# Kernel tuning notes

Measured on AMD Instinct MI355X. Metric: run time of the kernel, lower is better.

The kernel has to match this reference:

```python
import jax, jax.numpy as jnp
import numpy as np

HIDDEN = 1024
HEADS = 16
HEAD = HIDDEN // HEADS


def setup_inputs() -> dict:
    key = jax.random.key(0)
    ks = jax.random.split(key, 5)
    s = 1.0 / np.sqrt(HIDDEN)
    return {
        "x": jax.random.normal(ks[0], (32, 512, HIDDEN), dtype=jnp.float32),
        "w_qkv": jax.random.uniform(ks[1], (HIDDEN, 3 * HIDDEN), jnp.float32, -s, s),
        "b_qkv": jax.random.uniform(ks[2], (3 * HIDDEN,), jnp.float32, -s, s),
        "w_out": jax.random.uniform(ks[3], (HIDDEN, HIDDEN), jnp.float32, -s, s),
        "b_out": jax.random.uniform(ks[4], (HIDDEN,), jnp.float32, -s, s),
    }


def reference(x, w_qkv, b_qkv, w_out, b_out):
    bv, p, _ = x.shape
    qkv = x @ w_qkv + b_qkv                       # [bv, p, 3*hidden]
    qkv = qkv.reshape(bv, p, 3, HEADS, HEAD)
    q, k, v = qkv[:, :, 0], qkv[:, :, 1], qkv[:, :, 2]  # [bv, p, h, d]
    # scaled dot-product attention per head (dropout = identity in eval)
    scores = jnp.einsum("bqhd,bkhd->bhqk", q, k) / np.sqrt(HEAD).astype(np.float32)
    probs = jax.nn.softmax(scores, axis=-1)
    z = jnp.einsum("bhqk,bkhd->bqhd", probs, v).reshape(bv, p, HIDDEN)
    return z @ w_out + b_out
```

## Files before the change

### kernel.cpp

```cpp
#include <hip/hip_runtime.h>
#include <stdint.h>

#define KDIM 1024

typedef float  f32x4  __attribute__((ext_vector_type(4)));
typedef short  bf16x8 __attribute__((ext_vector_type(8)));
typedef unsigned short u16;
typedef unsigned int   u32;
typedef u16    u16x8  __attribute__((ext_vector_type(8)));

__device__ __forceinline__ float b2f(u16 u){ u32 x = ((u32)u)<<16; return __builtin_bit_cast(float, x); }
__device__ __forceinline__ u16  f2b(float f){
  u32 u = __builtin_bit_cast(u32, f);
  return (u16)((u + 0x7fffu + ((u>>16)&1u))>>16);
}
__device__ __forceinline__ u32 pk2(float a, float b){ return (u32)f2b(a) | ((u32)f2b(b)<<16); }

__device__ __forceinline__ void gload16(const void* g, void* l){
  __builtin_amdgcn_global_load_lds(
      (const __attribute__((address_space(1))) void*)g,
      (__attribute__((address_space(3))) void*)l, 16, 0, 0);
}

__global__ void k_cvt(const float* __restrict__ in, u16* __restrict__ out, int n8){
  int i = blockIdx.x*256 + threadIdx.x;
  if (i >= n8) return;
  const float4* p = (const float4*)in + (i<<1);
  float4 a = p[0], b = p[1];
  u16x8 o;
  o[0]=f2b(a.x); o[1]=f2b(a.y); o[2]=f2b(a.z); o[3]=f2b(a.w);
  o[4]=f2b(b.x); o[5]=f2b(b.y); o[6]=f2b(b.z); o[7]=f2b(b.w);
  *((u16x8*)out + i) = o;
}

__global__ void k_cvtT(const float* __restrict__ in, u16* __restrict__ out, int R, int C){
  __shared__ float t[32][33];
  int tx = threadIdx.x & 31, ty = threadIdx.x >> 5;
  int c0 = blockIdx.x<<5, r0 = blockIdx.y<<5;
  #pragma unroll
  for (int j=0;j<32;j+=8) t[ty+j][tx] = in[(r0+ty+j)*C + c0+tx];
  __syncthreads();
  #pragma unroll
  for (int j=0;j<32;j+=8) out[(c0+ty+j)*R + r0+tx] = f2b(t[tx][ty+j]);
}

template<int EPI>
__global__ __launch_bounds__(256, 3) void k_gemm(const u16* __restrict__ A, const u16* __restrict__ Bt,
    const float* __restrict__ bias, u16* __restrict__ oq, u16* __restrict__ ok2, u16* __restrict__ ov,
    float* __restrict__ of)
{
  __shared__ u16 lA[128*64];
  __shared__ u16 lB[128*64];
  const int t = threadIdx.x, lane = t & 63, wid = t >> 6;
  const int l15 = lane & 15, g = lane >> 4;
  const int m0 = blockIdx.y << 7, n0 = blockIdx.x << 7;
  const int wr = wid >> 1, wc = wid & 1;
  const f32x4 fz = {0.f,0.f,0.f,0.f};
  f32x4 acc[4][4];
  #pragma unroll
  for (int m=0;m<4;m++)
    #pragma unroll
    for (int n=0;n<4;n++) acc[m][n] = fz;

  for (int kt = 0; kt < KDIM; kt += 64) {
    __syncthreads();
    #pragma unroll
    for (int i=0;i<4;i++){
      int s = (i<<8) + t;
      int row = s >> 3;
      int c8 = (s & 7) ^ (row & 7);
      gload16(A + (m0 + row)*KDIM + kt + (c8<<3), (char*)lA + (((i<<2) + wid)<<10));
    }
    #pragma unroll
    for (int i=0;i<4;i++){
      int s = (i<<8) + t;
      int row = s >> 3;
      int c8 = (s & 7) ^ (row & 7);
      gload16(Bt + (n0 + row)*KDIM + kt + (c8<<3), (char*)lB + (((i<<2) + wid)<<10));
    }
    __syncthreads();
    #pragma unroll
    for (int ks=0; ks<2; ++ks){
      const int c8 = (ks<<2) + g;
      bf16x8 af[4], bfr[4];
      #pragma unroll
      for (int m=0;m<4;m++){
        int row = (wr<<6) + (m<<4) + l15;
        af[m] = *(const bf16x8*)((const char*)lA + (row<<7) + ((c8 ^ (row&7))<<4));
      }
      #pragma unroll
      for (int n=0;n<4;n++){
        int row = (wc<<6) + (n<<4) + l15;
        bfr[n] = *(const bf16x8*)((const char*)lB + (row<<7) + ((c8 ^ (row&7))<<4));
      }
      #pragma unroll
      for (int m=0;m<4;m++)
        #pragma unroll
        for (int n=0;n<4;n++)
          acc[m][n] = __builtin_amdgcn_mfma_f32_16x16x32_bf16(af[m], bfr[n], acc[m][n], 0,0,0);
    }
  }

  if (EPI == 0) {
    const int which = n0 >> 10;
    u16* dst = (which==0) ? oq : (which==1) ? ok2 : ov;
    #pragma unroll
    for (int n=0;n<4;n++){
      int n_g = n0 + (wc<<6) + (n<<4) + l15;
      float bv = bias[n_g];
      int h = (n_g >> 6) & 15, d = n_g & 63;
      #pragma unroll
      for (int m=0;m<4;m++){
        int mg = m0 + (wr<<6) + (m<<4) + (g<<2);
        #pragma unroll
        for (int j=0;j<4;j++){
          int m_g = mg + j;
          int bb = m_g >> 9, p = m_g & 511;
          dst[((bb*16 + h)*512 + p)*64 + d] = f2b(acc[m][n][j] + bv);
        }
      }
    }
  } else {
    #pragma unroll
    for (int n=0;n<4;n++){
      int n_g = n0 + (wc<<6) + (n<<4) + l15;
      float bv = bias[n_g];
      #pragma unroll
      for (int m=0;m<4;m++){
        int mg = m0 + (wr<<6) + (m<<4) + (g<<2);
        #pragma unroll
        for (int j=0;j<4;j++)
          of[(mg+j)*1024 + n_g] = acc[m][n][j] + bv;
      }
    }
  }
}

__global__ void k_vt(const u16* __restrict__ v, u16* __restrict__ vt){
  __shared__ u16 tl[64][65];
  const int bh = blockIdx.y, p0 = blockIdx.x << 6;
  const int t = threadIdx.x;
  #pragma unroll
  for (int i=0;i<4;i++){
    int e4 = (i<<8) + t;
    int r = e4 >> 4, c = (e4 & 15) << 2;
    ushort4 x = *(const ushort4*)&v[((bh<<9) + p0 + r)*64 + c];
    tl[r][c+0]=x.x; tl[r][c+1]=x.y; tl[r][c+2]=x.z; tl[r][c+3]=x.w;
  }
  __syncthreads();
  #pragma unroll
  for (int i=0;i<4;i++){
    int e4 = (i<<8) + t;
    int d = e4 >> 4, c = (e4 & 15) << 2;
    ushort4 x;
    x.x = tl[c+0][d]; x.y = tl[c+1][d]; x.z = tl[c+2][d]; x.w = tl[c+3][d];
    *(ushort4*)&vt[((bh<<6) + d)*512 + p0 + c] = x;
  }
}

__global__ __launch_bounds__(256, 2) void k_attn(const u16* __restrict__ q, const u16* __restrict__ k,
                                                 const u16* __restrict__ vt, u16* __restrict__ z)
{
  __shared__ u16 lK[64*64];
  __shared__ u16 lV[64*64];
  __shared__ u16 lP[4][64*64];
  const int t = threadIdx.x, lane = t & 63, wid = t >> 6;
  const int l15 = lane & 15, g = lane >> 4;
  const int bh = blockIdx.x >> 1, qt = blockIdx.x & 1;
  const int bb = bh >> 4, h = bh & 15;
  const int q0 = (qt<<8) + (wid<<6);
  const float cs = 0.18033688011112042f;

  bf16x8 qf[4][2];
  #pragma unroll
  for (int mf=0; mf<4; mf++)
    #pragma unroll
    for (int ks=0; ks<2; ks++){
      bf16x8 vq = *(const bf16x8*)(q + ((bh<<9) + q0 + (mf<<4) + l15)*64 + (ks<<5) + (g<<3));
      #pragma unroll
      for (int j=0;j<8;j++) vq[j] = (short)f2b(b2f((u16)vq[j]) * cs);
      qf[mf][ks] = vq;
    }

  const f32x4 fz = {0.f,0.f,0.f,0.f};
  f32x4 zt[4][4];
  #pragma unroll
  for (int df=0;df<4;df++)
    #pragma unroll
    for (int mf=0;mf<4;mf++) zt[df][mf] = fz;
  float mrun[4], lrun[4];
  #pragma unroll
  for (int mf=0;mf<4;mf++){ mrun[mf] = -__builtin_inff(); lrun[mf] = 0.f; }

  for (int kv0 = 0; kv0 < 512; kv0 += 64) {
    __syncthreads();
    #pragma unroll
    for (int i=0;i<2;i++){
      int s = (i<<8) + t;
      int row = s >> 3;
      int c8 = (s & 7) ^ (row & 7);
      gload16(k  + ((bh<<9) + kv0 + row)*64 + (c8<<3), (char*)lK + (((i<<2)+wid)<<10));
    }
    #pragma unroll
    for (int i=0;i<2;i++){
      int s = (i<<8) + t;
      int row = s >> 3;
      int c8 = (s & 7) ^ (row & 7);
      gload16(vt + ((bh<<6) + row)*512 + kv0 + (c8<<3), (char*)lV + (((i<<2)+wid)<<10));
    }
    __syncthreads();

    f32x4 sc[4][4];
    #pragma unroll
    for (int nf=0;nf<4;nf++)
      #pragma unroll
      for (int mf=0;mf<4;mf++) sc[nf][mf] = fz;
    #pragma unroll
    for (int ks=0; ks<2; ks++){
      const int c8 = (ks<<2) + g;
      bf16x8 kf[4];
      #pragma unroll
      for (int nf=0;nf<4;nf++){
        int row = (nf<<4) + l15;
        kf[nf] = *(const bf16x8*)((const char*)lK + (row<<7) + ((c8 ^ (row&7))<<4));
      }
      #pragma unroll
      for (int nf=0;nf<4;nf++)
        #pragma unroll
        for (int mf=0;mf<4;mf++)
          sc[nf][mf] = __builtin_amdgcn_mfma_f32_16x16x32_bf16(kf[nf], qf[mf][ks], sc[nf][mf], 0,0,0);
    }

    #pragma unroll
    for (int mf=0;mf<4;mf++){
      float pm = -__builtin_inff();
      #pragma unroll
      for (int nf=0;nf<4;nf++)
        #pragma unroll
        for (int j=0;j<4;j++) pm = fmaxf(pm, sc[nf][mf][j]);
      pm = fmaxf(pm, __shfl_xor(pm, 16));
      pm = fmaxf(pm, __shfl_xor(pm, 32));
      float mnew = fmaxf(mrun[mf], pm);
      float corr = __builtin_amdgcn_exp2f(mrun[mf] - mnew);
      mrun[mf] = mnew;
      float rs = 0.f;
      #pragma unroll
      for (int nf=0;nf<4;nf++)
        #pragma unroll
        for (int j=0;j<4;j++){
          float pv = __builtin_amdgcn_exp2f(sc[nf][mf][j] - mnew);
          sc[nf][mf][j] = pv; rs += pv;
        }
      rs += __shfl_xor(rs, 16);
      rs += __shfl_xor(rs, 32);
      lrun[mf] = lrun[mf]*corr + rs;
      #pragma unroll
      for (int df=0;df<4;df++){
        zt[df][mf][0]*=corr; zt[df][mf][1]*=corr; zt[df][mf][2]*=corr; zt[df][mf][3]*=corr;
      }
    }

    #pragma unroll
    for (int nf=0;nf<4;nf++)
      #pragma unroll
      for (int mf=0;mf<4;mf++){
        int qr = (mf<<4) + l15;
        int c8 = (nf<<1) + (g>>1);
        uint2 w2; w2.x = pk2(sc[nf][mf][0], sc[nf][mf][1]);
        w2.y = pk2(sc[nf][mf][2], sc[nf][mf][3]);
        *(uint2*)((char*)lP[wid] + (qr<<7) + ((c8 ^ (qr&7))<<4) + ((g&1)<<3)) = w2;
      }
    asm volatile("s_waitcnt lgkmcnt(0)" ::: "memory");

    #pragma unroll
    for (int ks=0; ks<2; ks++){
      const int c8 = (ks<<2) + g;
      bf16x8 vf[4], pf[4];
      #pragma unroll
      for (int df=0;df<4;df++){
        int row = (df<<4) + l15;
        vf[df] = *(const bf16x8*)((const char*)lV + (row<<7) + ((c8 ^ (row&7))<<4));
      }
      #pragma unroll
      for (int mf=0;mf<4;mf++){
        int qr = (mf<<4) + l15;
        pf[mf] = *(const bf16x8*)((const char*)lP[wid] + (qr<<7) + ((c8 ^ (qr&7))<<4));
      }
      #pragma unroll
      for (int df=0;df<4;df++)
        #pragma unroll
        for (int mf=0;mf<4;mf++)
          zt[df][mf] = __builtin_amdgcn_mfma_f32_16x16x32_bf16(vf[df], pf[mf], zt[df][mf], 0,0,0);
    }
  }

  #pragma unroll
  for (int mf=0;mf<4;mf++){
    float inv = 1.0f / lrun[mf];
    int qr = (mf<<4) + l15;
    int pg = (qt<<8) + (wid<<6) + qr;
    #pragma unroll
    for (int df=0;df<4;df++){
      int d0 = (df<<4) + (g<<2);
      ushort4 o;
      o.x = f2b(zt[df][mf][0]*inv);
      o.y = f2b(zt[df][mf][1]*inv);
      o.z = f2b(zt[df][mf][2]*inv);
      o.w = f2b(zt[df][mf][3]*inv);
      *(ushort4*)&z[ (((bb<<9) + pg)*16 + h)*64 + d0 ] = o;
    }
  }
}

extern "C" void kernel_launch(void* const* d_in, const int* in_sizes, int n_in,
                              void* d_out, int out_size, void* d_ws, size_t ws_size,
                              hipStream_t stream)
{
  (void)in_sizes; (void)n_in; (void)out_size; (void)ws_size;
  const float* x    = (const float*)d_in[0];
  const float* wqkv = (const float*)d_in[1];
  const float* bqkv = (const float*)d_in[2];
  const float* wout = (const float*)d_in[3];
  const float* bout = (const float*)d_in[4];
  float* out = (float*)d_out;
  char* w = (char*)d_ws;

  u16* wqT = (u16*)(w + 0);
  u16* woT = (u16*)(w + 6291456);
  u16* xb  = (u16*)(w + 8388608);
  u16* vtb = xb;
  u16* qb  = (u16*)(w + 41943040);
  u16* kb  = (u16*)(w + 75497472);
  u16* vb  = (u16*)(w + 109051904);
  u16* zb  = vb;

  k_cvt <<<dim3(8192),    dim3(256), 0, stream>>>(x, xb, 2097152);
  k_cvtT<<<dim3(96, 32),  dim3(256), 0, stream>>>(wqkv, wqT, 1024, 3072);
  k_cvtT<<<dim3(32, 32),  dim3(256), 0, stream>>>(wout, woT, 1024, 1024);
  k_gemm<0><<<dim3(24, 128), dim3(256), 0, stream>>>(xb, wqT, bqkv, qb, kb, vb, nullptr);
  k_vt  <<<dim3(8, 512),  dim3(256), 0, stream>>>(vb, vtb);
  k_attn<<<dim3(1024),    dim3(256), 0, stream>>>(qb, kb, vtb, zb);
  k_gemm<1><<<dim3(8, 128), dim3(256), 0, stream>>>(zb, woT, bout, nullptr, nullptr, nullptr, out);
}
```

Before: 377.4 us.

## Rewrite GEMM as 256x256 tile, 8-wave, double-buffered pipelined kernel

```diff
diff --git a/kernel.cpp b/kernel.cpp
--- a/kernel.cpp
+++ b/kernel.cpp
@@ -20,6 +20,14 @@
   __builtin_amdgcn_global_load_lds(
       (const __attribute__((address_space(1))) void*)g,
       (__attribute__((address_space(3))) void*)l, 16, 0, 0);
+}
+
+__device__ __forceinline__ void phase_bar(){
+  __builtin_amdgcn_sched_barrier(0);
+  asm volatile("s_waitcnt lgkmcnt(0)" ::: "memory");
+  __builtin_amdgcn_sched_barrier(0);
+  __builtin_amdgcn_s_barrier();
+  __builtin_amdgcn_sched_barrier(0);
 }
 
 __global__ void k_cvt(const float* __restrict__ in, u16* __restrict__ out, int n8){
@@ -44,93 +52,179 @@
   for (int j=0;j<32;j+=8) out[(c0+ty+j)*R + r0+tx] = f2b(t[tx][ty+j]);
 }
 
+__device__ __forceinline__ void stage2(const u16* __restrict__ src, int rowbase, int kt,
+                                       u16* lbuf, int grp0, int grp1, int lane){
+  int r7 = lane >> 3;
+  int c8 = (lane & 7) ^ r7;
+  const u16* s0 = src + (size_t)(rowbase + (grp0<<3) + r7)*KDIM + kt + (c8<<3);
+  const u16* s1 = src + (size_t)(rowbase + (grp1<<3) + r7)*KDIM + kt + (c8<<3);
+  gload16(s0, (char*)lbuf + (grp0<<10));
+  gload16(s1, (char*)lbuf + (grp1<<10));
+}
+
 template<int EPI>
-__global__ __launch_bounds__(256, 3) void k_gemm(const u16* __restrict__ A, const u16* __restrict__ Bt,
+__global__ __launch_bounds__(512, 2) void k_gemm(const u16* __restrict__ A, const u16* __restrict__ Bt,
     const float* __restrict__ bias, u16* __restrict__ oq, u16* __restrict__ ok2, u16* __restrict__ ov,
-    float* __restrict__ of)
+    float* __restrict__ of, int ntn)
 {
-  __shared__ u16 lA[128*64];
-  __shared__ u16 lB[128*64];
+  __shared__ u16 ldsb[2][2][256*64];
   const int t = threadIdx.x, lane = t & 63, wid = t >> 6;
   const int l15 = lane & 15, g = lane >> 4;
-  const int m0 = blockIdx.y << 7, n0 = blockIdx.x << 7;
-  const int wr = wid >> 1, wc = wid & 1;
+  const int wr = wid >> 2, wc = wid & 3;
+
+  const int nwg = gridDim.x, cpx = nwg >> 3, bid = blockIdx.x;
+  const int swz = (bid & 7)*cpx + (bid >> 3);
+  const int mt = swz / ntn, nt = swz % ntn;
+  const int m0 = mt << 8, n0 = nt << 8;
+
   const f32x4 fz = {0.f,0.f,0.f,0.f};
-  f32x4 acc[4][4];
-  #pragma unroll
-  for (int m=0;m<4;m++)
+  f32x4 acc[8][4];
+  #pragma unroll
+  for (int m=0;m<8;m++)
     #pragma unroll
     for (int n=0;n<4;n++) acc[m][n] = fz;
 
-  for (int kt = 0; kt < KDIM; kt += 64) {
-    __syncthreads();
-    #pragma unroll
-    for (int i=0;i<4;i++){
-      int s = (i<<8) + t;
-      int row = s >> 3;
-      int c8 = (s & 7) ^ (row & 7);
-      gload16(A + (m0 + row)*KDIM + kt + (c8<<3), (char*)lA + (((i<<2) + wid)<<10));
-    }
-    #pragma unroll
-    for (int i=0;i<4;i++){
-      int s = (i<<8) + t;
-      int row = s >> 3;
-      int c8 = (s & 7) ^ (row & 7);
-      gload16(Bt + (n0 + row)*KDIM + kt + (c8<<3), (char*)lB + (((i<<2) + wid)<<10));
-    }
-    __syncthreads();
-    #pragma unroll
-    for (int ks=0; ks<2; ++ks){
-      const int c8 = (ks<<2) + g;
-      bf16x8 af[4], bfr[4];
-      #pragma unroll
-      for (int m=0;m<4;m++){
-        int row = (wr<<6) + (m<<4) + l15;
-        af[m] = *(const bf16x8*)((const char*)lA + (row<<7) + ((c8 ^ (row&7))<<4));
-      }
-      #pragma unroll
-      for (int n=0;n<4;n++){
-        int row = (wc<<6) + (n<<4) + l15;
-        bfr[n] = *(const bf16x8*)((const char*)lB + (row<<7) + ((c8 ^ (row&7))<<4));
-      }
-      #pragma unroll
-      for (int m=0;m<4;m++)
-        #pragma unroll
-        for (int n=0;n<4;n++)
-          acc[m][n] = __builtin_amdgcn_mfma_f32_16x16x32_bf16(af[m], bfr[n], acc[m][n], 0,0,0);
-    }
+  const int NT = KDIM / 64;
+  const int sb0g0 = (wid<4)? wid    : wid+4;
+  const int sb0g1 = (wid<4)? wid+16 : wid+20;
+  const int sb1g0 = sb0g0 + 4, sb1g1 = sb0g1 + 4;
+
+  stage2(A,  m0, 0,  ldsb[0][0], wid,   wid+16, lane);
+  stage2(A,  m0, 0,  ldsb[0][0], wid+8, wid+24, lane);
+  stage2(Bt, n0, 0,  ldsb[0][1], sb0g0, sb0g1,  lane);
+  stage2(Bt, n0, 0,  ldsb[0][1], sb1g0, sb1g1,  lane);
+  stage2(A,  m0, 64, ldsb[1][0], wid,   wid+16, lane);
+  stage2(Bt, n0, 64, ldsb[1][1], sb0g0, sb0g1,  lane);
+  stage2(Bt, n0, 64, ldsb[1][1], sb1g0, sb1g1,  lane);
+  __builtin_amdgcn_sched_barrier(0);
+  asm volatile("s_waitcnt vmcnt(6) lgkmcnt(0)" ::: "memory");
+  __builtin_amdgcn_sched_barrier(0);
+  __builtin_amdgcn_s_barrier();
+  __builtin_amdgcn_sched_barrier(0);
+
+  for (int tt = 0; tt < NT; ++tt) {
+    const int b = tt & 1;
+    const char* cA = (const char*)ldsb[b][0];
+    const char* cB = (const char*)ldsb[b][1];
+    u16* nA1 = ldsb[b^1][0];
+    u16* nA2 = ldsb[b][0];
+    u16* nB2 = ldsb[b][1];
+    const int kt1 = (tt+1) << 6, kt2 = (tt+2) << 6;
+
+    bf16x8 af[4][2], b0[2][2], b1[2][2];
+
+    if (tt + 1 < NT) stage2(A, m0, kt1, nA1, wid+8, wid+24, lane);
+    #pragma unroll
+    for (int mf=0; mf<4; mf++)
+      #pragma unroll
+      for (int ks=0; ks<2; ks++){
+        int row = (wr<<7) + (mf<<4) + l15, c8 = (ks<<2) + g;
+        af[mf][ks] = *(const bf16x8*)(cA + (row<<7) + ((c8 ^ (row&7))<<4));
+      }
+    #pragma unroll
+    for (int nf=0; nf<2; nf++)
+      #pragma unroll
+      for (int ks=0; ks<2; ks++){
+        int row = (wc<<6) + (nf<<4) + l15, c8 = (ks<<2) + g;
+        b0[nf][ks] = *(const bf16x8*)(cB + (row<<7) + ((c8 ^ (row&7))<<4));
+      }
+    __builtin_amdgcn_s_setprio(1);
+    #pragma unroll
+    for (int mf=0; mf<4; mf++)
+      #pragma unroll
+      for (int nf=0; nf<2; nf++)
+        #pragma unroll
+        for (int ks=0; ks<2; ks++)
+          acc[mf][nf] = __builtin_amdgcn_mfma_f32_16x16x32_bf16(af[mf][ks], b0[nf][ks], acc[mf][nf], 0,0,0);
+    __builtin_amdgcn_s_setprio(0);
+    phase_bar();
+
+    if (tt + 2 < NT) stage2(A, m0, kt2, nA2, wid, wid+16, lane);
+    #pragma unroll
+    for (int nf=0; nf<2; nf++)
+      #pragma unroll
+      for (int ks=0; ks<2; ks++){
+        int row = (wc<<6) + ((nf+2)<<4) + l15, c8 = (ks<<2) + g;
+        b1[nf][ks] = *(const bf16x8*)(cB + (row<<7) + ((c8 ^ (row&7))<<4));
+      }
+    __builtin_amdgcn_s_setprio(1);
+    #pragma unroll
+    for (int mf=0; mf<4; mf++)
+      #pragma unroll
+      for (int nf=0; nf<2; nf++)
+        #pragma unroll
+        for (int ks=0; ks<2; ks++)
+          acc[mf][nf+2] = __builtin_amdgcn_mfma_f32_16x16x32_bf16(af[mf][ks], b1[nf][ks], acc[mf][nf+2], 0,0,0);
+    __builtin_amdgcn_s_setprio(0);
+    phase_bar();
+
+    if (tt + 2 < NT) stage2(Bt, n0, kt2, nB2, sb0g0, sb0g1, lane);
+    #pragma unroll
+    for (int mf=0; mf<4; mf++)
+      #pragma unroll
+      for (int ks=0; ks<2; ks++){
+        int row = (wr<<7) + ((mf+4)<<4) + l15, c8 = (ks<<2) + g;
+        af[mf][ks] = *(const bf16x8*)(cA + (row<<7) + ((c8 ^ (row&7))<<4));
+      }
+    __builtin_amdgcn_s_setprio(1);
+    #pragma unroll
+    for (int mf=0; mf<4; mf++)
+      #pragma unroll
+      for (int nf=0; nf<2; nf++)
+        #pragma unroll
+        for (int ks=0; ks<2; ks++)
+          acc[mf+4][nf] = __builtin_amdgcn_mfma_f32_16x16x32_bf16(af[mf][ks], b0[nf][ks], acc[mf+4][nf], 0,0,0);
+    __builtin_amdgcn_s_setprio(0);
+    phase_bar();
+
+    if (tt + 2 < NT) stage2(Bt, n0, kt2, nB2, sb1g0, sb1g1, lane);
+    __builtin_amdgcn_s_setprio(1);
+    #pragma unroll
+    for (int mf=0; mf<4; mf++)
+      #pragma unroll
+      for (int nf=0; nf<2; nf++)
+        #pragma unroll
+        for (int ks=0; ks<2; ks++)
+          acc[mf+4][nf+2] = __builtin_amdgcn_mfma_f32_16x16x32_bf16(af[mf][ks], b1[nf][ks], acc[mf+4][nf+2], 0,0,0);
+    __builtin_amdgcn_s_setprio(0);
+    __builtin_amdgcn_sched_barrier(0);
+    if (tt + 2 < NT) { asm volatile("s_waitcnt vmcnt(6) lgkmcnt(0)" ::: "memory"); }
+    else             { asm volatile("s_waitcnt vmcnt(0) lgkmcnt(0)" ::: "memory"); }
+    __builtin_amdgcn_sched_barrier(0);
+    __builtin_amdgcn_s_barrier();
+    __builtin_amdgcn_sched_barrier(0);
   }
 
   if (EPI == 0) {
     const int which = n0 >> 10;
     u16* dst = (which==0) ? oq : (which==1) ? ok2 : ov;
     #pragma unroll
-    for (int n=0;n<4;n++){
-      int n_g = n0 + (wc<<6) + (n<<4) + l15;
+    for (int nf=0; nf<4; nf++){
+      int n_g = n0 + (wc<<6) + (nf<<4) + l15;
       float bv = bias[n_g];
       int h = (n_g >> 6) & 15, d = n_g & 63;
       #pragma unroll
-      for (int m=0;m<4;m++){
-        int mg = m0 + (wr<<6) + (m<<4) + (g<<2);
+      for (int mf=0; mf<8; mf++){
+        int mg = m0 + (wr<<7) + (mf<<4) + (g<<2);
         #pragma unroll
         for (int j=0;j<4;j++){
           int m_g = mg + j;
           int bb = m_g >> 9, p = m_g & 511;
-          dst[((bb*16 + h)*512 + p)*64 + d] = f2b(acc[m][n][j] + bv);
+          dst[((bb*16 + h)*512 + p)*64 + d] = f2b(acc[mf][nf][j] + bv);
         }
       }
     }
   } else {
     #pragma unroll
-    for (int n=0;n<4;n++){
-      int n_g = n0 + (wc<<6) + (n<<4) + l15;
+    for (int nf=0; nf<4; nf++){
+      int n_g = n0 + (wc<<6) + (nf<<4) + l15;
       float bv = bias[n_g];
       #pragma unroll
-      for (int m=0;m<4;m++){
-        int mg = m0 + (wr<<6) + (m<<4) + (g<<2);
+      for (int mf=0; mf<8; mf++){
+        int mg = m0 + (wr<<7) + (mf<<4) + (g<<2);
         #pragma unroll
         for (int j=0;j<4;j++)
-          of[(mg+j)*1024 + n_g] = acc[m][n][j] + bv;
+          of[(size_t)(mg+j)*1024 + n_g] = acc[mf][nf][j] + bv;
       }
     }
   }
@@ -337,8 +431,8 @@
   k_cvt <<<dim3(8192),    dim3(256), 0, stream>>>(x, xb, 2097152);
   k_cvtT<<<dim3(96, 32),  dim3(256), 0, stream>>>(wqkv, wqT, 1024, 3072);
   k_cvtT<<<dim3(32, 32),  dim3(256), 0, stream>>>(wout, woT, 1024, 1024);
-  k_gemm<0><<<dim3(24, 128), dim3(256), 0, stream>>>(xb, wqT, bqkv, qb, kb, vb, nullptr);
+  k_gemm<0><<<dim3(768), dim3(512), 0, stream>>>(xb, wqT, bqkv, qb, kb, vb, nullptr, 12);
   k_vt  <<<dim3(8, 512),  dim3(256), 0, stream>>>(vb, vtb);
   k_attn<<<dim3(1024),    dim3(256), 0, stream>>>(qb, kb, vtb, zb);
-  k_gemm<1><<<dim3(8, 128), dim3(256), 0, stream>>>(zb, woT, bout, nullptr, nullptr, nullptr, out);
-}
+  k_gemm<1><<<dim3(256), dim3(512), 0, stream>>>(zb, woT, bout, nullptr, nullptr, nullptr, out, 4);
+}
```

New measurement: 386.5 us. 1.02x slower.

## Double-buffer K/V tiles in attention kernel to overlap loads with MFMA

Applied to the files above, without the earlier changes.

```diff
diff --git a/kernel.cpp b/kernel.cpp
--- a/kernel.cpp
+++ b/kernel.cpp
@@ -20,6 +20,14 @@
   __builtin_amdgcn_global_load_lds(
       (const __attribute__((address_space(1))) void*)g,
       (__attribute__((address_space(3))) void*)l, 16, 0, 0);
+}
+
+__device__ __forceinline__ void tile_fence(){
+  __builtin_amdgcn_sched_barrier(0);
+  asm volatile("s_waitcnt vmcnt(0) lgkmcnt(0)" ::: "memory");
+  __builtin_amdgcn_sched_barrier(0);
+  __builtin_amdgcn_s_barrier();
+  __builtin_amdgcn_sched_barrier(0);
 }
 
 __global__ void k_cvt(const float* __restrict__ in, u16* __restrict__ out, int n8){
@@ -161,8 +169,8 @@
 __global__ __launch_bounds__(256, 2) void k_attn(const u16* __restrict__ q, const u16* __restrict__ k,
                                                  const u16* __restrict__ vt, u16* __restrict__ z)
 {
-  __shared__ u16 lK[64*64];
-  __shared__ u16 lV[64*64];
+  __shared__ u16 lK[2][64*64];
+  __shared__ u16 lV[2][64*64];
   __shared__ u16 lP[4][64*64];
   const int t = threadIdx.x, lane = t & 63, wid = t >> 6;
   const int l15 = lane & 15, g = lane >> 4;
@@ -192,23 +200,31 @@
   #pragma unroll
   for (int mf=0;mf<4;mf++){ mrun[mf] = -__builtin_inff(); lrun[mf] = 0.f; }
 
-  for (int kv0 = 0; kv0 < 512; kv0 += 64) {
-    __syncthreads();
+  auto stage_kv = [&](int kv0, int bufIdx){
     #pragma unroll
     for (int i=0;i<2;i++){
       int s = (i<<8) + t;
       int row = s >> 3;
       int c8 = (s & 7) ^ (row & 7);
-      gload16(k  + ((bh<<9) + kv0 + row)*64 + (c8<<3), (char*)lK + (((i<<2)+wid)<<10));
+      gload16(k  + ((bh<<9) + kv0 + row)*64 + (c8<<3), (char*)lK[bufIdx] + (((i<<2)+wid)<<10));
     }
     #pragma unroll
     for (int i=0;i<2;i++){
       int s = (i<<8) + t;
       int row = s >> 3;
       int c8 = (s & 7) ^ (row & 7);
-      gload16(vt + ((bh<<6) + row)*512 + kv0 + (c8<<3), (char*)lV + (((i<<2)+wid)<<10));
-    }
-    __syncthreads();
+      gload16(vt + ((bh<<6) + row)*512 + kv0 + (c8<<3), (char*)lV[bufIdx] + (((i<<2)+wid)<<10));
+    }
+  };
+
+  stage_kv(0, 0);
+  tile_fence();
+
+  for (int it = 0; it < 8; ++it) {
+    const int cur = it & 1;
+    const char* cK = (const char*)lK[cur];
+    const char* cV = (const char*)lV[cur];
+    if (it + 1 < 8) stage_kv((it + 1) << 6, cur ^ 1);
 
     f32x4 sc[4][4];
     #pragma unroll
@@ -222,7 +238,7 @@
       #pragma unroll
       for (int nf=0;nf<4;nf++){
         int row = (nf<<4) + l15;
-        kf[nf] = *(const bf16x8*)((const char*)lK + (row<<7) + ((c8 ^ (row&7))<<4));
+        kf[nf] = *(const bf16x8*)(cK + (row<<7) + ((c8 ^ (row&7))<<4));
       }
       #pragma unroll
       for (int nf=0;nf<4;nf++)
@@ -270,7 +286,9 @@
         w2.y = pk2(sc[nf][mf][2], sc[nf][mf][3]);
         *(uint2*)((char*)lP[wid] + (qr<<7) + ((c8 ^ (qr&7))<<4) + ((g&1)<<3)) = w2;
       }
+    __builtin_amdgcn_sched_barrier(0);
     asm volatile("s_waitcnt lgkmcnt(0)" ::: "memory");
+    __builtin_amdgcn_sched_barrier(0);
 
     #pragma unroll
     for (int ks=0; ks<2; ks++){
@@ -279,7 +297,7 @@
       #pragma unroll
       for (int df=0;df<4;df++){
         int row = (df<<4) + l15;
-        vf[df] = *(const bf16x8*)((const char*)lV + (row<<7) + ((c8 ^ (row&7))<<4));
+        vf[df] = *(const bf16x8*)(cV + (row<<7) + ((c8 ^ (row&7))<<4));
       }
       #pragma unroll
       for (int mf=0;mf<4;mf++){
@@ -292,6 +310,8 @@
         for (int mf=0;mf<4;mf++)
           zt[df][mf] = __builtin_amdgcn_mfma_f32_16x16x32_bf16(vf[df], pf[mf], zt[df][mf], 0,0,0);
     }
+
+    tile_fence();
   }
 
   #pragma unroll
```

Result: faster. 369.7 us (-2.0%).
